# Performance work log

Hardware: AMD Instinct MI355X
Metric: run time of the kernel (lower is better)

The kernel has to match this reference:

```python
import jax, jax.numpy as jnp
import numpy as np

H = 256          # hidden_size
S = 4            # feature size (2D -> 4)
T_OUT = 16       # args.output // args.skip
HT_LIM = 100.0   # hardtanh limit
B = 16384
OBS = 16


def lstm_cell(x, h, c, Wih, Whh, bih, bhh):
    # PyTorch gate order: i, f, g, o
    g = x @ Wih.T + h @ Whh.T + bih + bhh  # [B, 4H]
    i, f, gg, o = jnp.split(g, 4, axis=-1)
    c = jax.nn.sigmoid(f) * c + jax.nn.sigmoid(i) * jnp.tanh(gg)
    h = jax.nn.sigmoid(o) * jnp.tanh(c)
    return h, c


def encode(seq, Wih, Whh, bih, bhh):
    # seq: [B, T, S]; single-layer LSTM, return final (h, c)
    h0 = jnp.zeros((seq.shape[0], H), seq.dtype)
    def step(carry, x):
        h, c = carry
        return lstm_cell(x, h, c, Wih, Whh, bih, bhh), None
    (h, c), _ = jax.lax.scan(step, (h0, h0), jnp.swapaxes(seq, 0, 1))
    return h, c


def setup_inputs() -> dict:
    key = jax.random.key(0)
    ks = jax.random.split(key, 32)
    sc = 0.05
    def W(k, shape):
        return (jax.random.normal(k, shape, jnp.float32) * sc)
    inp = {
        'speed': jax.random.normal(ks[0], (B, OBS, S), jnp.float32),
        'pos': jax.random.normal(ks[1], (B, OBS, S), jnp.float32),
        # speed encoder LSTM
        'sp_Wih': W(ks[2], (4 * H, S)), 'sp_Whh': W(ks[3], (4 * H, H)),
        'sp_bih': W(ks[4], (4 * H,)), 'sp_bhh': W(ks[5], (4 * H,)),
        # pos encoder LSTM
        'po_Wih': W(ks[6], (4 * H, S)), 'po_Whh': W(ks[7], (4 * H, H)),
        'po_bih': W(ks[8], (4 * H,)), 'po_bhh': W(ks[9], (4 * H,)),
        # speed decoder LSTMCell
        'dsp_Wih': W(ks[10], (4 * H, S)), 'dsp_Whh': W(ks[11], (4 * H, H)),
        'dsp_bih': W(ks[12], (4 * H,)), 'dsp_bhh': W(ks[13], (4 * H,)),
        # crossing decoder LSTMCell
        'dcr_Wih': W(ks[14], (4 * H, S)), 'dcr_Whh': W(ks[15], (4 * H, H)),
        'dcr_bih': W(ks[16], (4 * H,)), 'dcr_bhh': W(ks[17], (4 * H,)),
        # heads
        'fc_speed_W': W(ks[18], (S, H)), 'fc_speed_b': W(ks[19], (S,)),
        'fc_cross_W': W(ks[20], (2, H)), 'fc_cross_b': W(ks[21], (2,)),
        'emb_W': W(ks[22], (S, H)), 'emb_b': W(ks[23], (S,)),
    }
    return inp


def reference(speed, pos,
              sp_Wih, sp_Whh, sp_bih, sp_bhh,
              po_Wih, po_Whh, po_bih, po_bhh,
              dsp_Wih, dsp_Whh, dsp_bih, dsp_bhh,
              dcr_Wih, dcr_Whh, dcr_bih, dcr_bhh,
              fc_speed_W, fc_speed_b, fc_cross_W, fc_cross_b,
              emb_W, emb_b):
    hsp, csp = encode(speed, sp_Wih, sp_Whh, sp_bih, sp_bhh)
    hpo, cpo = encode(pos, po_Wih, po_Whh, po_bih, po_bhh)
    h0 = hpo + hsp
    c0 = cpo + csp

    # ---- speed decoder: feed back hardtanh(fc_speed(h)) (detached) ----
    def sp_step(carry, _):
        h, c, x = carry
        h, c = lstm_cell(x, h, c, dsp_Wih, dsp_Whh, dsp_bih, dsp_bhh)
        out = jnp.clip(h @ fc_speed_W.T + fc_speed_b, -HT_LIM, HT_LIM)
        return (h, c, jax.lax.stop_gradient(out)), out
    _, sp_outs = jax.lax.scan(sp_step, (h0, c0, speed[:, -1, :]), None, length=T_OUT)
    speed_outputs = jnp.swapaxes(sp_outs, 0, 1)  # [B, T_OUT, S]

    # ---- crossing decoder: feed back relu(pos_embedding(h)) (detached) ----
    def cr_step(carry, _):
        h, c, x = carry
        h, c = lstm_cell(x, h, c, dcr_Wih, dcr_Whh, dcr_bih, dcr_bhh)
        logits = jax.nn.relu(h @ fc_cross_W.T + fc_cross_b)  # [B, 2]
        out = jax.nn.softmax(logits, axis=1)
        x_next = jax.lax.stop_gradient(jax.nn.relu(h @ emb_W.T + emb_b))
        return (h, c, x_next), out
    _, cr_outs = jax.lax.scan(cr_step, (h0, c0, pos[:, -1, :]), None, length=T_OUT)
    crossing_outputs = jnp.swapaxes(cr_outs, 0, 1)  # [B, T_OUT, 2]

    return (speed_outputs, crossing_outputs)
```

## Files before the change

### kernel.cpp

```cpp
#include <hip/hip_runtime.h>

typedef unsigned short ushort_t;
typedef __bf16 bf16x8 __attribute__((ext_vector_type(8)));
typedef float f32x4 __attribute__((ext_vector_type(4)));

#define PACK_W_ELEMS (8*9*8*512)
#define HEAD_ELEMS   (9*512)
#define PACK_TOTAL   (4*PACK_W_ELEMS + 2*HEAD_ELEMS)
#define FLAG_OFS     PACK_TOTAL

__device__ __forceinline__ float bf2f(ushort_t u){ return __uint_as_float(((unsigned)u)<<16); }
__device__ __forceinline__ ushort_t f2bf(float f){
  __bf16 h = (__bf16)f;
  return *(ushort_t*)&h;
}
__device__ __forceinline__ float rcp_(float x){ return __builtin_amdgcn_rcpf(x); }
__device__ __forceinline__ float sigmf_(float x){ return rcp_(1.0f + __expf(-x)); }
__device__ __forceinline__ float tanhf_(float x){ return 1.0f - 2.0f*rcp_(1.0f + __expf(2.0f*x)); }

__device__ __forceinline__ int sniff_f32(const ushort_t* w){
  int f32 = 0;
  #pragma unroll
  for (int i = 0; i < 32; ++i){
    float f = bf2f(w[2*i]);
    if (!(f > -8.f && f < 8.f)) f32 = 1;
  }
  return f32;
}
__device__ __forceinline__ float ldin(const ushort_t* p, int i, int f32){
  return f32 ? ((const float*)p)[i] : bf2f(p[i]);
}
__device__ __forceinline__ ushort_t ldw(const ushort_t* p, int i, int f32){
  return f32 ? f2bf(((const float*)p)[i]) : p[i];
}

struct PackArgs {
  const ushort_t* wih[4]; const ushort_t* whh[4];
  const ushort_t* bih[4]; const ushort_t* bhh[4];
  const ushort_t* fcsp_w; const ushort_t* fcsp_b;
  const ushort_t* fccr_w; const ushort_t* fccr_b;
  const ushort_t* emb_w;  const ushort_t* emb_b;
  ushort_t* ws;
};

__global__ void pack_kernel(PackArgs a){
  const int f32 = sniff_f32(a.whh[0]);
  int idx = blockIdx.x*256 + threadIdx.x;
  if (blockIdx.x == 0 && threadIdx.x == 0) *(int*)(a.ws + FLAG_OFS) = f32;
  const int total_w = 4*PACK_W_ELEMS;
  if (idx < total_w){
    int l = idx / PACK_W_ELEMS;
    int r = idx % PACK_W_ELEMS;
    int j = r & 7;
    int lane = (r>>3) & 63;
    int tile = r >> 9;
    int gu = tile & 7;
    int kt = (tile >> 3) % 9;
    int wv = tile / 72;
    int g = gu >> 1, u = gu & 1;
    int n = (g*16 + wv*2 + u)*16 + (lane & 15);
    int k = kt*32 + ((lane>>4)<<3) + j;
    ushort_t v = 0;
    if (k < 256)       v = ldw(a.whh[l], n*256 + k, f32);
    else if (k < 260)  v = ldw(a.wih[l], n*4 + (k-256), f32);
    else if (k == 260) v = f2bf(ldin(a.bih[l], n, f32) + ldin(a.bhh[l], n, f32));
    a.ws[l*PACK_W_ELEMS + r] = v;
    return;
  }
  idx -= total_w;
  if (idx < 2*HEAD_ELEMS){
    int which = idx / HEAD_ELEMS;
    int r = idx % HEAD_ELEMS;
    int j = r & 7; int lane = (r>>3)&63; int kt = r>>9;
    int n = lane & 15; int k = kt*32 + ((lane>>4)<<3) + j;
    ushort_t v = 0;
    if (which == 0){
      if (n < 4){
        if (k < 256)       v = ldw(a.fcsp_w, n*256 + k, f32);
        else if (k == 260) v = f2bf(ldin(a.fcsp_b, n, f32));
      }
    } else {
      if (n < 4){
        if (k < 256)       v = ldw(a.emb_w, n*256 + k, f32);
        else if (k == 260) v = f2bf(ldin(a.emb_b, n, f32));
      } else if (n < 6){
        if (k < 256)       v = ldw(a.fccr_w, (n-4)*256 + k, f32);
        else if (k == 260) v = f2bf(ldin(a.fccr_b, n-4, f32));
      }
    }
    a.ws[total_w + idx] = v;
  }
}

__device__ __forceinline__ void gate_gemm(const ushort_t* __restrict__ Aln,
                                          const ushort_t* __restrict__ bw,
                                          f32x4 (&acc)[4][8], int lane){
  #pragma unroll
  for (int i = 0; i < 4; ++i)
    #pragma unroll
    for (int j = 0; j < 8; ++j) acc[i][j] = (f32x4){0.f,0.f,0.f,0.f};
  bf16x8 p0 = *(const bf16x8*)&bw[0*512];
  bf16x8 p1 = *(const bf16x8*)&bw[1*512];
  bf16x8 p2 = *(const bf16x8*)&bw[2*512];
  bf16x8 p3 = *(const bf16x8*)&bw[3*512];
  const ushort_t* bp = bw;
  #pragma unroll 1
  for (int kt = 0; kt < 9; ++kt){
    bf16x8 q0 = *(const bf16x8*)&bp[4*512];
    bf16x8 q1 = *(const bf16x8*)&bp[5*512];
    bf16x8 q2 = *(const bf16x8*)&bp[6*512];
    bf16x8 q3 = *(const bf16x8*)&bp[7*512];
    bf16x8 a0 = *(const bf16x8*)&Aln[(0*9+kt)*512];
    bf16x8 a1 = *(const bf16x8*)&Aln[(1*9+kt)*512];
    bf16x8 a2 = *(const bf16x8*)&Aln[(2*9+kt)*512];
    bf16x8 a3 = *(const bf16x8*)&Aln[(3*9+kt)*512];
    acc[0][0] = __builtin_amdgcn_mfma_f32_16x16x32_bf16(a0, p0, acc[0][0], 0, 0, 0);
    acc[1][0] = __builtin_amdgcn_mfma_f32_16x16x32_bf16(a1, p0, acc[1][0], 0, 0, 0);
    acc[2][0] = __builtin_amdgcn_mfma_f32_16x16x32_bf16(a2, p0, acc[2][0], 0, 0, 0);
    acc[3][0] = __builtin_amdgcn_mfma_f32_16x16x32_bf16(a3, p0, acc[3][0], 0, 0, 0);
    acc[0][1] = __builtin_amdgcn_mfma_f32_16x16x32_bf16(a0, p1, acc[0][1], 0, 0, 0);
    acc[1][1] = __builtin_amdgcn_mfma_f32_16x16x32_bf16(a1, p1, acc[1][1], 0, 0, 0);
    acc[2][1] = __builtin_amdgcn_mfma_f32_16x16x32_bf16(a2, p1, acc[2][1], 0, 0, 0);
    acc[3][1] = __builtin_amdgcn_mfma_f32_16x16x32_bf16(a3, p1, acc[3][1], 0, 0, 0);
    acc[0][2] = __builtin_amdgcn_mfma_f32_16x16x32_bf16(a0, p2, acc[0][2], 0, 0, 0);
    acc[1][2] = __builtin_amdgcn_mfma_f32_16x16x32_bf16(a1, p2, acc[1][2], 0, 0, 0);
    acc[2][2] = __builtin_amdgcn_mfma_f32_16x16x32_bf16(a2, p2, acc[2][2], 0, 0, 0);
    acc[3][2] = __builtin_amdgcn_mfma_f32_16x16x32_bf16(a3, p2, acc[3][2], 0, 0, 0);
    acc[0][3] = __builtin_amdgcn_mfma_f32_16x16x32_bf16(a0, p3, acc[0][3], 0, 0, 0);
    acc[1][3] = __builtin_amdgcn_mfma_f32_16x16x32_bf16(a1, p3, acc[1][3], 0, 0, 0);
    acc[2][3] = __builtin_amdgcn_mfma_f32_16x16x32_bf16(a2, p3, acc[2][3], 0, 0, 0);
    acc[3][3] = __builtin_amdgcn_mfma_f32_16x16x32_bf16(a3, p3, acc[3][3], 0, 0, 0);
    if (kt < 8){
      p0 = *(const bf16x8*)&bp[4096 + 0*512];
      p1 = *(const bf16x8*)&bp[4096 + 1*512];
      p2 = *(const bf16x8*)&bp[4096 + 2*512];
      p3 = *(const bf16x8*)&bp[4096 + 3*512];
    }
    acc[0][4] = __builtin_amdgcn_mfma_f32_16x16x32_bf16(a0, q0, acc[0][4], 0, 0, 0);
    acc[1][4] = __builtin_amdgcn_mfma_f32_16x16x32_bf16(a1, q0, acc[1][4], 0, 0, 0);
    acc[2][4] = __builtin_amdgcn_mfma_f32_16x16x32_bf16(a2, q0, acc[2][4], 0, 0, 0);
    acc[3][4] = __builtin_amdgcn_mfma_f32_16x16x32_bf16(a3, q0, acc[3][4], 0, 0, 0);
    acc[0][5] = __builtin_amdgcn_mfma_f32_16x16x32_bf16(a0, q1, acc[0][5], 0, 0, 0);
    acc[1][5] = __builtin_amdgcn_mfma_f32_16x16x32_bf16(a1, q1, acc[1][5], 0, 0, 0);
    acc[2][5] = __builtin_amdgcn_mfma_f32_16x16x32_bf16(a2, q1, acc[2][5], 0, 0, 0);
    acc[3][5] = __builtin_amdgcn_mfma_f32_16x16x32_bf16(a3, q1, acc[3][5], 0, 0, 0);
    acc[0][6] = __builtin_amdgcn_mfma_f32_16x16x32_bf16(a0, q2, acc[0][6], 0, 0, 0);
    acc[1][6] = __builtin_amdgcn_mfma_f32_16x16x32_bf16(a1, q2, acc[1][6], 0, 0, 0);
    acc[2][6] = __builtin_amdgcn_mfma_f32_16x16x32_bf16(a2, q2, acc[2][6], 0, 0, 0);
    acc[3][6] = __builtin_amdgcn_mfma_f32_16x16x32_bf16(a3, q2, acc[3][6], 0, 0, 0);
    acc[0][7] = __builtin_amdgcn_mfma_f32_16x16x32_bf16(a0, q3, acc[0][7], 0, 0, 0);
    acc[1][7] = __builtin_amdgcn_mfma_f32_16x16x32_bf16(a1, q3, acc[1][7], 0, 0, 0);
    acc[2][7] = __builtin_amdgcn_mfma_f32_16x16x32_bf16(a2, q3, acc[2][7], 0, 0, 0);
    acc[3][7] = __builtin_amdgcn_mfma_f32_16x16x32_bf16(a3, q3, acc[3][7], 0, 0, 0);
    bp += 4096;
  }
}

__device__ __forceinline__ void gates_wb(f32x4 (&acc)[4][8], float (&cw)[4][2][4],
                                         ushort_t* __restrict__ Ap, int wbBase){
  #pragma unroll
  for (int mt = 0; mt < 4; ++mt)
    #pragma unroll
    for (int u = 0; u < 2; ++u)
      #pragma unroll
      for (int r = 0; r < 4; ++r){
        float cn = sigmf_(acc[mt][2+u][r])*cw[mt][u][r]
                 + sigmf_(acc[mt][u][r])*tanhf_(acc[mt][4+u][r]);
        float hn = sigmf_(acc[mt][6+u][r])*tanhf_(cn);
        cw[mt][u][r] = cn;
        Ap[mt*4608 + u*256 + r*8 + wbBase] = f2bf(hn);
      }
}

__global__ __launch_bounds__(512, 2) void pvlstm_main(
    const ushort_t* __restrict__ ws,
    const ushort_t* __restrict__ speed,
    const ushort_t* __restrict__ pos,
    void* __restrict__ outv)
{
  __shared__ ushort_t ApS[4*9*512];
  __shared__ ushort_t ApP[4*9*512];
  __shared__ ushort_t xsS[64*64];
  __shared__ ushort_t xsP[64*64];
  __shared__ float    ostS[64*64];
  __shared__ float    ostC[64*32];

  const int f32   = *(const int*)(ws + FLAG_OFS);
  const int tid   = threadIdx.x;
  const int lane  = tid & 63;
  const int w     = tid >> 6;
  const int col16 = lane & 15;
  const int quad  = lane >> 4;
  const int brow0 = blockIdx.x * 64;
  const int wbBase = w*512 + (col16>>3)*128 + quad*32 + (col16&7);

  ushort_t* outu = (ushort_t*)outv;
  float*    outf = (float*)outv;

  const ushort_t* headsp = ws + 4*PACK_W_ELEMS;
  const ushort_t* headcr = headsp + HEAD_ELEMS;
  const ushort_t* aS  = ApS + lane*8;
  const ushort_t* aP  = ApP + lane*8;
  const ushort_t* bwS  = ws + 0*PACK_W_ELEMS + (size_t)w*36864 + (size_t)lane*8;
  const ushort_t* bwP  = ws + 1*PACK_W_ELEMS + (size_t)w*36864 + (size_t)lane*8;
  const ushort_t* bwDS = ws + 2*PACK_W_ELEMS + (size_t)w*36864 + (size_t)lane*8;
  const ushort_t* bwDC = ws + 3*PACK_W_ELEMS + (size_t)w*36864 + (size_t)lane*8;

  float cwA[4][2][4], cwB[4][2][4];
  f32x4 acc[4][8];

  for (int i = tid; i < 4096; i += 512){
    int gi = (brow0 + (i>>6))*64 + (i&63);
    xsS[i] = f2bf(ldin(speed, gi, f32));
    xsP[i] = f2bf(ldin(pos,   gi, f32));
  }
  for (int i = tid; i < 4*9*512/2; i += 512){
    ((unsigned*)ApS)[i] = 0u; ((unsigned*)ApP)[i] = 0u;
  }
  #pragma unroll
  for (int mt = 0; mt < 4; ++mt)
    #pragma unroll
    for (int u = 0; u < 2; ++u)
      #pragma unroll
      for (int r = 0; r < 4; ++r){ cwA[mt][u][r] = 0.f; cwB[mt][u][r] = 0.f; }
  __syncthreads();
  if (tid < 64){
    ushort_t* xpS = &ApS[((tid>>4)*9 + 8)*512 + (tid&15)*8];
    ushort_t* xpP = &ApP[((tid>>4)*9 + 8)*512 + (tid&15)*8];
    *(uint2*)xpS = *(const uint2*)&xsS[tid*64];
    xpS[4] = (ushort_t)0x3f80;
    xpP[4] = (ushort_t)0x3f80;
  }
  __syncthreads();

  for (int t = 0; t < 16; ++t){
    if (t > 0) gates_wb(acc, cwB, ApP, wbBase);
    if (tid < 64)
      *(uint2*)&ApP[((tid>>4)*9 + 8)*512 + (tid&15)*8] = *(const uint2*)&xsP[tid*64 + t*4];
    gate_gemm(aS, bwS, acc, lane);
    __syncthreads();
    gates_wb(acc, cwA, ApS, wbBase);
    if (t < 15 && tid < 64)
      *(uint2*)&ApS[((tid>>4)*9 + 8)*512 + (tid&15)*8] = *(const uint2*)&xsS[tid*64 + t*4 + 4];
    gate_gemm(aP, bwP, acc, lane);
    __syncthreads();
  }
  #pragma unroll
  for (int mt = 0; mt < 4; ++mt)
    #pragma unroll
    for (int u = 0; u < 2; ++u)
      #pragma unroll
      for (int r = 0; r < 4; ++r){
        float cn = sigmf_(acc[mt][2+u][r])*cwB[mt][u][r]
                 + sigmf_(acc[mt][u][r])*tanhf_(acc[mt][4+u][r]);
        float hn = sigmf_(acc[mt][6+u][r])*tanhf_(cn);
        float c0 = cwA[mt][u][r] + cn;
        cwA[mt][u][r] = c0; cwB[mt][u][r] = c0;
        const int ad = mt*4608 + u*256 + r*8 + wbBase;
        ushort_t h0 = f2bf(bf2f(ApS[ad]) + hn);
        ApS[ad] = h0; ApP[ad] = h0;
      }
  if (tid < 64){
    *(uint2*)&ApS[((tid>>4)*9 + 8)*512 + (tid&15)*8] = *(const uint2*)&xsS[tid*64 + 60];
    *(uint2*)&ApP[((tid>>4)*9 + 8)*512 + (tid&15)*8] = *(const uint2*)&xsP[tid*64 + 60];
  }
  __syncthreads();

  for (int t = 0; t < 16; ++t){
    if (t > 0 && w >= 4){
      const int mt = w - 4;
      f32x4 hacc = (f32x4){0.f,0.f,0.f,0.f};
      #pragma unroll
      for (int kt = 0; kt < 9; ++kt){
        bf16x8 a  = *(const bf16x8*)&aP[(mt*9+kt)*512];
        bf16x8 bv = *(const bf16x8*)&headcr[((size_t)kt*64 + lane)*8];
        hacc = __builtin_amdgcn_mfma_f32_16x16x32_bf16(a, bv, hacc, 0, 0, 0);
      }
      const int s = col16;
      #pragma unroll
      for (int r = 0; r < 4; ++r){
        float v = fmaxf(hacc[r], 0.f);
        const float o = __shfl_xor(v, 1, 64);
        const int m = mt*16 + quad*4 + r;
        if (s < 4){
          ApP[(mt*9+8)*512 + (m&15)*8 + s] = f2bf(v);
        } else if (s < 6){
          const float mx = fmaxf(v, o);
          const float e0 = __expf(v-mx), e1 = __expf(o-mx);
          ostC[m*32 + (t-1)*2 + (s-4)] = e0*rcp_(e0+e1);
        }
      }
    }
    gate_gemm(aS, bwDS, acc, lane);
    __syncthreads();
    gates_wb(acc, cwA, ApS, wbBase);
    gate_gemm(aP, bwDC, acc, lane);
    __syncthreads();
    gates_wb(acc, cwB, ApP, wbBase);
    if (w < 4){
      const int mt = w;
      f32x4 hacc = (f32x4){0.f,0.f,0.f,0.f};
      #pragma unroll
      for (int kt = 0; kt < 9; ++kt){
        bf16x8 a  = *(const bf16x8*)&aS[(mt*9+kt)*512];
        bf16x8 bv = *(const bf16x8*)&headsp[((size_t)kt*64 + lane)*8];
        hacc = __builtin_amdgcn_mfma_f32_16x16x32_bf16(a, bv, hacc, 0, 0, 0);
      }
      const int s = col16;
      if (s < 4){
        #pragma unroll
        for (int r = 0; r < 4; ++r){
          float v = fminf(fmaxf(hacc[r], -100.f), 100.f);
          const int m = mt*16 + quad*4 + r;
          ostS[m*64 + t*4 + s] = v;
          ApS[(mt*9+8)*512 + (m&15)*8 + s] = f2bf(v);
        }
      }
    }
    __syncthreads();
  }
  if (w >= 4){
    const int mt = w - 4;
    f32x4 hacc = (f32x4){0.f,0.f,0.f,0.f};
    #pragma unroll
    for (int kt = 0; kt < 9; ++kt){
      bf16x8 a  = *(const bf16x8*)&aP[(mt*9+kt)*512];
      bf16x8 bv = *(const bf16x8*)&headcr[((size_t)kt*64 + lane)*8];
      hacc = __builtin_amdgcn_mfma_f32_16x16x32_bf16(a, bv, hacc, 0, 0, 0);
    }
    const int s = col16;
    if (s >= 4 && s < 6){
      #pragma unroll
      for (int r = 0; r < 4; ++r){
        float v = fmaxf(hacc[r], 0.f);
        const float o = __shfl_xor(v, 1, 64);
        const int m = mt*16 + quad*4 + r;
        const float mx = fmaxf(v, o);
        const float e0 = __expf(v-mx), e1 = __expf(o-mx);
        ostC[m*32 + 15*2 + (s-4)] = e0*rcp_(e0+e1);
      }
    }
  }
  __syncthreads();

  for (int i = tid; i < 4096; i += 512){
    const int oi = (brow0 + (i>>6))*64 + (i&63);
    const float v = ostS[i];
    if (f32) outf[oi] = v; else outu[oi] = f2bf(v);
  }
  for (int i = tid; i < 2048; i += 512){
    const int oi = 1048576 + (brow0 + (i>>5))*32 + (i&31);
    const float v = ostC[i];
    if (f32) outf[oi] = v; else outu[oi] = f2bf(v);
  }
}

extern "C" void kernel_launch(void* const* d_in, const int* in_sizes, int n_in,
                              void* d_out, int out_size, void* d_ws, size_t ws_size,
                              hipStream_t stream) {
  PackArgs pa;
  pa.wih[0]=(const ushort_t*)d_in[2];  pa.whh[0]=(const ushort_t*)d_in[3];
  pa.bih[0]=(const ushort_t*)d_in[4];  pa.bhh[0]=(const ushort_t*)d_in[5];
  pa.wih[1]=(const ushort_t*)d_in[6];  pa.whh[1]=(const ushort_t*)d_in[7];
  pa.bih[1]=(const ushort_t*)d_in[8];  pa.bhh[1]=(const ushort_t*)d_in[9];
  pa.wih[2]=(const ushort_t*)d_in[10]; pa.whh[2]=(const ushort_t*)d_in[11];
  pa.bih[2]=(const ushort_t*)d_in[12]; pa.bhh[2]=(const ushort_t*)d_in[13];
  pa.wih[3]=(const ushort_t*)d_in[14]; pa.whh[3]=(const ushort_t*)d_in[15];
  pa.bih[3]=(const ushort_t*)d_in[16]; pa.bhh[3]=(const ushort_t*)d_in[17];
  pa.fcsp_w=(const ushort_t*)d_in[18]; pa.fcsp_b=(const ushort_t*)d_in[19];
  pa.fccr_w=(const ushort_t*)d_in[20]; pa.fccr_b=(const ushort_t*)d_in[21];
  pa.emb_w =(const ushort_t*)d_in[22]; pa.emb_b =(const ushort_t*)d_in[23];
  pa.ws = (ushort_t*)d_ws;

  hipLaunchKernelGGL(pack_kernel, dim3((PACK_TOTAL + 255)/256), dim3(256), 0, stream, pa);
  hipLaunchKernelGGL(pvlstm_main, dim3(256), dim3(512), 0, stream,
      (const ushort_t*)d_ws,
      (const ushort_t*)d_in[0], (const ushort_t*)d_in[1],
      d_out);
}
```

Measured before the change: 851.8 us.

## Split gate GEMM into two half-width passes to halve accumulator registers

The per-wave gate GEMM is split into two passes, each computing 4 of the 8 accumulator column tiles (one hidden unit slice u at a time). The LSTM cell update runs right after each pass, and h values are held in registers until after the barrier. This halves the live f32 accumulator footprint (128 to 64 VGPRs) to relieve register pressure at 2 waves per SIMD. In exchange the A fragments are reloaded from LDS twice and the weight loads are restructured with a strided layout. Input loads and output stores also switch to nontemporal hints.

Result: slower. 1.039 ms (+22.0%).

```diff
diff --git a/kernel.cpp b/kernel.cpp
--- a/kernel.cpp
+++ b/kernel.cpp
@@ -29,6 +29,10 @@
 }
 __device__ __forceinline__ float ldin(const ushort_t* p, int i, int f32){
   return f32 ? ((const float*)p)[i] : bf2f(p[i]);
+}
+__device__ __forceinline__ float ldin_nt(const ushort_t* p, int i, int f32){
+  return f32 ? __builtin_nontemporal_load((const float*)p + i)
+             : bf2f(__builtin_nontemporal_load(p + i));
 }
 __device__ __forceinline__ ushort_t ldw(const ushort_t* p, int i, int f32){
   return f32 ? f2bf(((const float*)p)[i]) : p[i];
@@ -92,84 +96,76 @@
   }
 }
 
-__device__ __forceinline__ void gate_gemm(const ushort_t* __restrict__ Aln,
-                                          const ushort_t* __restrict__ bw,
-                                          f32x4 (&acc)[4][8], int lane){
+__device__ __forceinline__ void gate_gemm_u(const ushort_t* __restrict__ Aln,
+                                            const ushort_t* __restrict__ bwu,
+                                            f32x4 (&a4)[4][4]){
   #pragma unroll
   for (int i = 0; i < 4; ++i)
     #pragma unroll
-    for (int j = 0; j < 8; ++j) acc[i][j] = (f32x4){0.f,0.f,0.f,0.f};
-  bf16x8 p0 = *(const bf16x8*)&bw[0*512];
-  bf16x8 p1 = *(const bf16x8*)&bw[1*512];
-  bf16x8 p2 = *(const bf16x8*)&bw[2*512];
-  bf16x8 p3 = *(const bf16x8*)&bw[3*512];
-  const ushort_t* bp = bw;
+    for (int j = 0; j < 4; ++j) a4[i][j] = (f32x4){0.f,0.f,0.f,0.f};
+  bf16x8 p0 = *(const bf16x8*)&bwu[0*1024];
+  bf16x8 p1 = *(const bf16x8*)&bwu[1*1024];
+  bf16x8 p2 = *(const bf16x8*)&bwu[2*1024];
+  bf16x8 p3 = *(const bf16x8*)&bwu[3*1024];
+  const ushort_t* bp = bwu;
   #pragma unroll 1
   for (int kt = 0; kt < 9; ++kt){
-    bf16x8 q0 = *(const bf16x8*)&bp[4*512];
-    bf16x8 q1 = *(const bf16x8*)&bp[5*512];
-    bf16x8 q2 = *(const bf16x8*)&bp[6*512];
-    bf16x8 q3 = *(const bf16x8*)&bp[7*512];
     bf16x8 a0 = *(const bf16x8*)&Aln[(0*9+kt)*512];
     bf16x8 a1 = *(const bf16x8*)&Aln[(1*9+kt)*512];
     bf16x8 a2 = *(const bf16x8*)&Aln[(2*9+kt)*512];
     bf16x8 a3 = *(const bf16x8*)&Aln[(3*9+kt)*512];
-    acc[0][0] = __builtin_amdgcn_mfma_f32_16x16x32_bf16(a0, p0, acc[0][0], 0, 0, 0);
-    acc[1][0] = __builtin_amdgcn_mfma_f32_16x16x32_bf16(a1, p0, acc[1][0], 0, 0, 0);
-    acc[2][0] = __builtin_amdgcn_mfma_f32_16x16x32_bf16(a2, p0, acc[2][0], 0, 0, 0);
-    acc[3][0] = __builtin_amdgcn_mfma_f32_16x16x32_bf16(a3, p0, acc[3][0], 0, 0, 0);
-    acc[0][1] = __builtin_amdgcn_mfma_f32_16x16x32_bf16(a0, p1, acc[0][1], 0, 0, 0);
-    acc[1][1] = __builtin_amdgcn_mfma_f32_16x16x32_bf16(a1, p1, acc[1][1], 0, 0, 0);
-    acc[2][1] = __builtin_amdgcn_mfma_f32_16x16x32_bf16(a2, p1, acc[2][1], 0, 0, 0);
-    acc[3][1] = __builtin_amdgcn_mfma_f32_16x16x32_bf16(a3, p1, acc[3][1], 0, 0, 0);
-    acc[0][2] = __builtin_amdgcn_mfma_f32_16x16x32_bf16(a0, p2, acc[0][2], 0, 0, 0);
-    acc[1][2] = __builtin_amdgcn_mfma_f32_16x16x32_bf16(a1, p2, acc[1][2], 0, 0, 0);
-    acc[2][2] = __builtin_amdgcn_mfma_f32_16x16x32_bf16(a2, p2, acc[2][2], 0, 0, 0);
-    acc[3][2] = __builtin_amdgcn_mfma_f32_16x16x32_bf16(a3, p2, acc[3][2], 0, 0, 0);
-    acc[0][3] = __builtin_amdgcn_mfma_f32_16x16x32_bf16(a0, p3, acc[0][3], 0, 0, 0);
-    acc[1][3] = __builtin_amdgcn_mfma_f32_16x16x32_bf16(a1, p3, acc[1][3], 0, 0, 0);
-    acc[2][3] = __builtin_amdgcn_mfma_f32_16x16x32_bf16(a2, p3, acc[2][3], 0, 0, 0);
-    acc[3][3] = __builtin_amdgcn_mfma_f32_16x16x32_bf16(a3, p3, acc[3][3], 0, 0, 0);
+    a4[0][0] = __builtin_amdgcn_mfma_f32_16x16x32_bf16(a0, p0, a4[0][0], 0, 0, 0);
+    a4[1][0] = __builtin_amdgcn_mfma_f32_16x16x32_bf16(a1, p0, a4[1][0], 0, 0, 0);
+    a4[2][0] = __builtin_amdgcn_mfma_f32_16x16x32_bf16(a2, p0, a4[2][0], 0, 0, 0);
+    a4[3][0] = __builtin_amdgcn_mfma_f32_16x16x32_bf16(a3, p0, a4[3][0], 0, 0, 0);
+    a4[0][1] = __builtin_amdgcn_mfma_f32_16x16x32_bf16(a0, p1, a4[0][1], 0, 0, 0);
+    a4[1][1] = __builtin_amdgcn_mfma_f32_16x16x32_bf16(a1, p1, a4[1][1], 0, 0, 0);
+    a4[2][1] = __builtin_amdgcn_mfma_f32_16x16x32_bf16(a2, p1, a4[2][1], 0, 0, 0);
+    a4[3][1] = __builtin_amdgcn_mfma_f32_16x16x32_bf16(a3, p1, a4[3][1], 0, 0, 0);
+    bf16x8 q0, q1, q2, q3;
     if (kt < 8){
-      p0 = *(const bf16x8*)&bp[4096 + 0*512];
-      p1 = *(const bf16x8*)&bp[4096 + 1*512];
-      p2 = *(const bf16x8*)&bp[4096 + 2*512];
-      p3 = *(const bf16x8*)&bp[4096 + 3*512];
-    }
-    acc[0][4] = __builtin_amdgcn_mfma_f32_16x16x32_bf16(a0, q0, acc[0][4], 0, 0, 0);
-    acc[1][4] = __builtin_amdgcn_mfma_f32_16x16x32_bf16(a1, q0, acc[1][4], 0, 0, 0);
-    acc[2][4] = __builtin_amdgcn_mfma_f32_16x16x32_bf16(a2, q0, acc[2][4], 0, 0, 0);
-    acc[3][4] = __builtin_amdgcn_mfma_f32_16x16x32_bf16(a3, q0, acc[3][4], 0, 0, 0);
-    acc[0][5] = __builtin_amdgcn_mfma_f32_16x16x32_bf16(a0, q1, acc[0][5], 0, 0, 0);
-    acc[1][5] = __builtin_amdgcn_mfma_f32_16x16x32_bf16(a1, q1, acc[1][5], 0, 0, 0);
-    acc[2][5] = __builtin_amdgcn_mfma_f32_16x16x32_bf16(a2, q1, acc[2][5], 0, 0, 0);
-    acc[3][5] = __builtin_amdgcn_mfma_f32_16x16x32_bf16(a3, q1, acc[3][5], 0, 0, 0);
-    acc[0][6] = __builtin_amdgcn_mfma_f32_16x16x32_bf16(a0, q2, acc[0][6], 0, 0, 0);
-    acc[1][6] = __builtin_amdgcn_mfma_f32_16x16x32_bf16(a1, q2, acc[1][6], 0, 0, 0);
-    acc[2][6] = __builtin_amdgcn_mfma_f32_16x16x32_bf16(a2, q2, acc[2][6], 0, 0, 0);
-    acc[3][6] = __builtin_amdgcn_mfma_f32_16x16x32_bf16(a3, q2, acc[3][6], 0, 0, 0);
-    acc[0][7] = __builtin_amdgcn_mfma_f32_16x16x32_bf16(a0, q3, acc[0][7], 0, 0, 0);
-    acc[1][7] = __builtin_amdgcn_mfma_f32_16x16x32_bf16(a1, q3, acc[1][7], 0, 0, 0);
-    acc[2][7] = __builtin_amdgcn_mfma_f32_16x16x32_bf16(a2, q3, acc[2][7], 0, 0, 0);
-    acc[3][7] = __builtin_amdgcn_mfma_f32_16x16x32_bf16(a3, q3, acc[3][7], 0, 0, 0);
+      q0 = *(const bf16x8*)&bp[4096 + 0*1024];
+      q1 = *(const bf16x8*)&bp[4096 + 1*1024];
+      q2 = *(const bf16x8*)&bp[4096 + 2*1024];
+      q3 = *(const bf16x8*)&bp[4096 + 3*1024];
+    }
+    a4[0][2] = __builtin_amdgcn_mfma_f32_16x16x32_bf16(a0, p2, a4[0][2], 0, 0, 0);
+    a4[1][2] = __builtin_amdgcn_mfma_f32_16x16x32_bf16(a1, p2, a4[1][2], 0, 0, 0);
+    a4[2][2] = __builtin_amdgcn_mfma_f32_16x16x32_bf16(a2, p2, a4[2][2], 0, 0, 0);
+    a4[3][2] = __builtin_amdgcn_mfma_f32_16x16x32_bf16(a3, p2, a4[3][2], 0, 0, 0);
+    a4[0][3] = __builtin_amdgcn_mfma_f32_16x16x32_bf16(a0, p3, a4[0][3], 0, 0, 0);
+    a4[1][3] = __builtin_amdgcn_mfma_f32_16x16x32_bf16(a1, p3, a4[1][3], 0, 0, 0);
+    a4[2][3] = __builtin_amdgcn_mfma_f32_16x16x32_bf16(a2, p3, a4[2][3], 0, 0, 0);
+    a4[3][3] = __builtin_amdgcn_mfma_f32_16x16x32_bf16(a3, p3, a4[3][3], 0, 0, 0);
+    if (kt < 8){ p0 = q0; p1 = q1; p2 = q2; p3 = q3; }
     bp += 4096;
   }
 }
 
-__device__ __forceinline__ void gates_wb(f32x4 (&acc)[4][8], float (&cw)[4][2][4],
-                                         ushort_t* __restrict__ Ap, int wbBase){
+template<int U>
+__device__ __forceinline__ void wbcalc(const f32x4 (&a4)[4][4], float (&cw)[4][2][4],
+                                       float (&hn)[2][4][4]){
   #pragma unroll
   for (int mt = 0; mt < 4; ++mt)
     #pragma unroll
+    for (int r = 0; r < 4; ++r){
+      float cn = sigmf_(a4[mt][1][r])*cw[mt][U][r]
+               + sigmf_(a4[mt][0][r])*tanhf_(a4[mt][2][r]);
+      float h  = sigmf_(a4[mt][3][r])*tanhf_(cn);
+      cw[mt][U][r] = cn;
+      hn[U][mt][r] = h;
+    }
+}
+
+__device__ __forceinline__ void store_hn(ushort_t* __restrict__ Ap, const float (&hn)[2][4][4],
+                                         int wbBase){
+  #pragma unroll
+  for (int mt = 0; mt < 4; ++mt)
+    #pragma unroll
     for (int u = 0; u < 2; ++u)
       #pragma unroll
-      for (int r = 0; r < 4; ++r){
-        float cn = sigmf_(acc[mt][2+u][r])*cw[mt][u][r]
-                 + sigmf_(acc[mt][u][r])*tanhf_(acc[mt][4+u][r]);
-        float hn = sigmf_(acc[mt][6+u][r])*tanhf_(cn);
-        cw[mt][u][r] = cn;
-        Ap[mt*4608 + u*256 + r*8 + wbBase] = f2bf(hn);
-      }
+      for (int r = 0; r < 4; ++r)
+        Ap[mt*4608 + u*256 + r*8 + wbBase] = f2bf(hn[u][mt][r]);
 }
 
 __global__ __launch_bounds__(512, 2) void pvlstm_main(
@@ -201,18 +197,16 @@
   const ushort_t* headcr = headsp + HEAD_ELEMS;
   const ushort_t* aS  = ApS + lane*8;
   const ushort_t* aP  = ApP + lane*8;
-  const ushort_t* bwS  = ws + 0*PACK_W_ELEMS + (size_t)w*36864 + (size_t)lane*8;
-  const ushort_t* bwP  = ws + 1*PACK_W_ELEMS + (size_t)w*36864 + (size_t)lane*8;
-  const ushort_t* bwDS = ws + 2*PACK_W_ELEMS + (size_t)w*36864 + (size_t)lane*8;
-  const ushort_t* bwDC = ws + 3*PACK_W_ELEMS + (size_t)w*36864 + (size_t)lane*8;
+  const ushort_t* bwB = ws + (unsigned)(w*36864 + lane*8);
 
   float cwA[4][2][4], cwB[4][2][4];
-  f32x4 acc[4][8];
+  float hnS[2][4][4], hnP[2][4][4];
+  f32x4 a4[4][4];
 
   for (int i = tid; i < 4096; i += 512){
     int gi = (brow0 + (i>>6))*64 + (i&63);
-    xsS[i] = f2bf(ldin(speed, gi, f32));
-    xsP[i] = f2bf(ldin(pos,   gi, f32));
+    xsS[i] = f2bf(ldin_nt(speed, gi, f32));
+    xsP[i] = f2bf(ldin_nt(pos,   gi, f32));
   }
   for (int i = tid; i < 4*9*512/2; i += 512){
     ((unsigned*)ApS)[i] = 0u; ((unsigned*)ApP)[i] = 0u;
@@ -234,15 +228,17 @@
   __syncthreads();
 
   for (int t = 0; t < 16; ++t){
-    if (t > 0) gates_wb(acc, cwB, ApP, wbBase);
+    if (t > 0) store_hn(ApP, hnP, wbBase);
     if (tid < 64)
       *(uint2*)&ApP[((tid>>4)*9 + 8)*512 + (tid&15)*8] = *(const uint2*)&xsP[tid*64 + t*4];
-    gate_gemm(aS, bwS, acc, lane);
-    __syncthreads();
-    gates_wb(acc, cwA, ApS, wbBase);
+    gate_gemm_u(aS, bwB + 0*PACK_W_ELEMS,       a4);  wbcalc<0>(a4, cwA, hnS);
+    gate_gemm_u(aS, bwB + 0*PACK_W_ELEMS + 512, a4);  wbcalc<1>(a4, cwA, hnS);
+    __syncthreads();
+    store_hn(ApS, hnS, wbBase);
     if (t < 15 && tid < 64)
       *(uint2*)&ApS[((tid>>4)*9 + 8)*512 + (tid&15)*8] = *(const uint2*)&xsS[tid*64 + t*4 + 4];
-    gate_gemm(aP, bwP, acc, lane);
+    gate_gemm_u(aP, bwB + 1*PACK_W_ELEMS,       a4);  wbcalc<0>(a4, cwB, hnP);
+    gate_gemm_u(aP, bwB + 1*PACK_W_ELEMS + 512, a4);  wbcalc<1>(a4, cwB, hnP);
     __syncthreads();
   }
   #pragma unroll
@@ -251,13 +247,10 @@
     for (int u = 0; u < 2; ++u)
       #pragma unroll
       for (int r = 0; r < 4; ++r){
-        float cn = sigmf_(acc[mt][2+u][r])*cwB[mt][u][r]
-                 + sigmf_(acc[mt][u][r])*tanhf_(acc[mt][4+u][r]);
-        float hn = sigmf_(acc[mt][6+u][r])*tanhf_(cn);
-        float c0 = cwA[mt][u][r] + cn;
+        float c0 = cwA[mt][u][r] + cwB[mt][u][r];
         cwA[mt][u][r] = c0; cwB[mt][u][r] = c0;
         const int ad = mt*4608 + u*256 + r*8 + wbBase;
-        ushort_t h0 = f2bf(bf2f(ApS[ad]) + hn);
+        ushort_t h0 = f2bf(bf2f(ApS[ad]) + hnP[u][mt][r]);
         ApS[ad] = h0; ApP[ad] = h0;
       }
   if (tid < 64){
@@ -291,12 +284,14 @@
         }
       }
     }
-    gate_gemm(aS, bwDS, acc, lane);
-    __syncthreads();
-    gates_wb(acc, cwA, ApS, wbBase);
-    gate_gemm(aP, bwDC, acc, lane);
-    __syncthreads();
-    gates_wb(acc, cwB, ApP, wbBase);
+    gate_gemm_u(aS, bwB + 2*PACK_W_ELEMS,       a4);  wbcalc<0>(a4, cwA, hnS);
+    gate_gemm_u(aS, bwB + 2*PACK_W_ELEMS + 512, a4);  wbcalc<1>(a4, cwA, hnS);
+    __syncthreads();
+    store_hn(ApS, hnS, wbBase);
+    gate_gemm_u(aP, bwB + 3*PACK_W_ELEMS,       a4);  wbcalc<0>(a4, cwB, hnP);
+    gate_gemm_u(aP, bwB + 3*PACK_W_ELEMS + 512, a4);  wbcalc<1>(a4, cwB, hnP);
+    __syncthreads();
+    store_hn(ApP, hnP, wbBase);
     if (w < 4){
       const int mt = w;
       f32x4 hacc = (f32x4){0.f,0.f,0.f,0.f};
@@ -346,12 +341,14 @@
   for (int i = tid; i < 4096; i += 512){
     const int oi = (brow0 + (i>>6))*64 + (i&63);
     const float v = ostS[i];
-    if (f32) outf[oi] = v; else outu[oi] = f2bf(v);
+    if (f32) __builtin_nontemporal_store(v, outf + oi);
+    else     __builtin_nontemporal_store(f2bf(v), outu + oi);
   }
   for (int i = tid; i < 2048; i += 512){
     const int oi = 1048576 + (brow0 + (i>>5))*32 + (i&31);
     const float v = ostC[i];
-    if (f32) outf[oi] = v; else outu[oi] = f2bf(v);
+    if (f32) __builtin_nontemporal_store(v, outf + oi);
+    else     __builtin_nontemporal_store(f2bf(v), outu + oi);
   }
 }
 
```
